# Optimization experiments

Hardware: AMD Instinct MI355X
Metric: run time of the kernel (lower is better)

## Reference

```python
import jax, jax.numpy as jnp
import numpy as np

BS = 4
N_NODES = 10000
N_FEAT = 64
HID = 128
N_LAYERS = 4
HID_FC = 512
N_CLASSES = 10
N_EDGES = 160000


def setup_inputs() -> dict:
    key = jax.random.key(0)
    ks = jax.random.split(key, 10)
    x = jax.random.normal(ks[0], (BS, N_NODES, N_FEAT), jnp.float32)
    edge_index = jax.random.randint(ks[1], (2, N_EDGES), 0, N_NODES, dtype=jnp.int32)
    # batch[b*N_NODES + i] = b, matching x.view(num_nodes*bs, -1) row-major flatten
    batch = jnp.repeat(jnp.arange(BS, dtype=jnp.int32), N_NODES)
    W1 = jax.random.normal(ks[2], (N_FEAT, HID), jnp.float32) * (N_FEAT ** -0.5)
    b1 = jax.random.normal(ks[3], (HID,), jnp.float32) * 0.01
    Ws = jax.random.normal(ks[4], (N_LAYERS - 1, HID, HID), jnp.float32) * (HID ** -0.5)
    bconvs = jax.random.normal(ks[5], (N_LAYERS - 1, HID), jnp.float32) * 0.01
    lin1_w = jax.random.normal(ks[6], (N_LAYERS * HID, HID_FC), jnp.float32) * ((N_LAYERS * HID) ** -0.5)
    lin1_b = jax.random.normal(ks[7], (HID_FC,), jnp.float32) * 0.01
    lin2_w = jax.random.normal(ks[8], (HID_FC, N_CLASSES), jnp.float32) * (HID_FC ** -0.5)
    lin2_b = jax.random.normal(ks[9], (N_CLASSES,), jnp.float32) * 0.01
    return {"x": x, "edge_index": edge_index, "batch": batch,
            "W1": W1, "b1": b1, "Ws": Ws, "bconvs": bconvs,
            "lin1_w": lin1_w, "lin1_b": lin1_b, "lin2_w": lin2_w, "lin2_b": lin2_b}


def _gcn_norm(edge_index, n):
    # PyG GCNConv: add self-loops, symmetric normalization D^-1/2 (A+I) D^-1/2
    loops = jnp.arange(n, dtype=edge_index.dtype)
    src = jnp.concatenate([edge_index[0], loops])
    dst = jnp.concatenate([edge_index[1], loops])
    deg = jnp.zeros((n,), jnp.float32).at[dst].add(1.0)
    dinv = jnp.where(deg > 0, jax.lax.rsqrt(deg), 0.0)
    return src, dst, dinv[src] * dinv[dst]


def reference(x, edge_index, batch, W1, b1, Ws, bconvs, lin1_w, lin1_b, lin2_w, lin2_b):
    bs, n, _ = x.shape
    src, dst, norm = _gcn_norm(edge_index, n)

    def gcn(h, W, b):
        m = (h @ W)[:, src, :] * norm[None, :, None]          # [bs, E+n, H]
        agg = jax.vmap(lambda mm: jax.ops.segment_sum(mm, dst, num_segments=n))(m)
        return agg + b

    h = jax.nn.relu(gcn(x, W1, b1))
    xs = [h]
    for i in range(Ws.shape[0]):
        h = jax.nn.relu(gcn(h, Ws[i], bconvs[i]))
        xs.append(h)
    # torch.stack(xs, -1).view(bs, n, -1): per-channel layer interleave
    h = jnp.stack(xs, -1).reshape(bs, n, -1)                   # [bs, n, L*H]
    flat = h.reshape(bs * n, -1)
    summed = jax.ops.segment_sum(flat, batch, num_segments=bs)
    counts = jax.ops.segment_sum(jnp.ones((bs * n,), flat.dtype), batch, num_segments=bs)
    pooled = summed / counts[:, None]                          # global_mean_pool
    h = jax.nn.relu(pooled @ lin1_w + lin1_b)
    # dropout p=0.5 is inference-disabled (training=False)
    logits = h @ lin2_w + lin2_b
    return jax.nn.log_softmax(logits, axis=-1)
```

## Files before the change

### kernel.cpp

```cpp
#include <hip/hip_runtime.h>
#include <hip/hip_bf16.h>
#include <math.h>

#define N_NODES 10000
#define N_EDGES 160000
#define BS      4
#define N_TOT   (BS * N_NODES)
#define HID     128
#define NPC     4
#define CHUNKS  (N_NODES/NPC)
#define SLOTS   2500
#define HID_FC  512
#define N_CLASSES 10
#define N_LAYERS  4
#define DEG_CAP 64
#define ZERO_INT4 325000

using bf16x8 = __attribute__((ext_vector_type(8))) short;
using f32x4  = __attribute__((ext_vector_type(4))) float;
using f32x2  = __attribute__((ext_vector_type(2))) float;

__device__ __forceinline__ unsigned bf_rne(float x) {
    unsigned b = __float_as_uint(x);
    return (b + 0x7fffu + ((b >> 16) & 1u)) >> 16;
}
__device__ __forceinline__ float bf2f(unsigned hi16) { return __uint_as_float(hi16 << 16); }

#if __has_builtin(__builtin_amdgcn_cvt_pk_f32_fp8) && __has_builtin(__builtin_amdgcn_cvt_pk_fp8_f32)
#define HW_FP8 1
#else
#define HW_FP8 0
#endif

__device__ __forceinline__ float fp8_dec1(unsigned b) {
    unsigned s = (b & 0x80u) << 24;
    unsigned em = b & 0x7Fu;
    float mag;
    if (em >= 8u) mag = __uint_as_float((((em >> 3) + 120u) << 23) | ((em & 7u) << 20));
    else          mag = (float)em * 0x1p-9f;
    return __uint_as_float(s | __float_as_uint(mag));
}

__device__ __forceinline__ unsigned fp8_enc(float x) {
#if HW_FP8
    return (unsigned)(__builtin_amdgcn_cvt_pk_fp8_f32(x, x, 0, false) & 0xFF);
#else
    unsigned s = (__float_as_uint(x) >> 24) & 0x80u;
    float ax = fabsf(x);
    unsigned r;
    if (ax >= 0x1p-6f) {
        if (ax > 448.f) r = 0x7Eu;
        else {
            unsigned b = __float_as_uint(ax);
            unsigned t = b + 0x7FFFFu + ((b >> 20) & 1u);
            r = (t >> 20) - 960u;
        }
    } else {
        r = (unsigned)__float2int_rn(ax * 512.f);
    }
    return s | r;
#endif
}

__device__ __forceinline__ void fp8x8_dec(uint2 u, float* f) {
#if HW_FP8
    f32x2 p0 = __builtin_amdgcn_cvt_pk_f32_fp8((int)u.x, false);
    f32x2 p1 = __builtin_amdgcn_cvt_pk_f32_fp8((int)u.x, true);
    f32x2 p2 = __builtin_amdgcn_cvt_pk_f32_fp8((int)u.y, false);
    f32x2 p3 = __builtin_amdgcn_cvt_pk_f32_fp8((int)u.y, true);
    f[0] = p0[0]; f[1] = p0[1]; f[2] = p1[0]; f[3] = p1[1];
    f[4] = p2[0]; f[5] = p2[1]; f[6] = p3[0]; f[7] = p3[1];
#else
    f[0] = fp8_dec1(u.x & 0xFFu);         f[1] = fp8_dec1((u.x >> 8) & 0xFFu);
    f[2] = fp8_dec1((u.x >> 16) & 0xFFu); f[3] = fp8_dec1((u.x >> 24) & 0xFFu);
    f[4] = fp8_dec1(u.y & 0xFFu);         f[5] = fp8_dec1((u.y >> 8) & 0xFFu);
    f[6] = fp8_dec1((u.y >> 16) & 0xFFu); f[7] = fp8_dec1((u.y >> 24) & 0xFFu);
#endif
}

__device__ __forceinline__ void agg_node(const uint2* __restrict__ tin,
                                         const int* __restrict__ counts,
                                         const int2* __restrict__ csr,
                                         int n, int l, const float* bvv, float* r) {
    int cnt = counts[n];
    const float dn = rsqrtf((float)(cnt + 1));
    if (cnt > DEG_CAP) cnt = DEG_CAP;
    const int no = (cnt + 7) >> 3;
    float acc[8];
    {
        uint2 us = tin[n * 64 + l];
        float sf[8];
        fp8x8_dec(us, sf);
        #pragma unroll
        for (int j = 0; j < 8; ++j) acc[j] = dn * sf[j];
    }
    const int4* cp = (const int4*)(csr + ((size_t)n << 6));
    for (int q = 0; q < no; ++q) {
        int4 q0 = cp[4 * q], q1 = cp[4 * q + 1], q2 = cp[4 * q + 2], q3 = cp[4 * q + 3];
        uint2 u0 = tin[q0.x * 64 + l];
        uint2 u1 = tin[q0.z * 64 + l];
        uint2 u2 = tin[q1.x * 64 + l];
        uint2 u3 = tin[q1.z * 64 + l];
        uint2 u4 = tin[q2.x * 64 + l];
        uint2 u5 = tin[q2.z * 64 + l];
        uint2 u6 = tin[q3.x * 64 + l];
        uint2 u7 = tin[q3.z * 64 + l];
        float w0 = __int_as_float(q0.y), w1 = __int_as_float(q0.w);
        float w2 = __int_as_float(q1.y), w3 = __int_as_float(q1.w);
        float w4 = __int_as_float(q2.y), w5 = __int_as_float(q2.w);
        float w6 = __int_as_float(q3.y), w7 = __int_as_float(q3.w);
        float f[8];
        fp8x8_dec(u0, f);
        #pragma unroll
        for (int j = 0; j < 8; ++j) acc[j] = fmaf(w0, f[j], acc[j]);
        fp8x8_dec(u1, f);
        #pragma unroll
        for (int j = 0; j < 8; ++j) acc[j] = fmaf(w1, f[j], acc[j]);
        fp8x8_dec(u2, f);
        #pragma unroll
        for (int j = 0; j < 8; ++j) acc[j] = fmaf(w2, f[j], acc[j]);
        fp8x8_dec(u3, f);
        #pragma unroll
        for (int j = 0; j < 8; ++j) acc[j] = fmaf(w3, f[j], acc[j]);
        fp8x8_dec(u4, f);
        #pragma unroll
        for (int j = 0; j < 8; ++j) acc[j] = fmaf(w4, f[j], acc[j]);
        fp8x8_dec(u5, f);
        #pragma unroll
        for (int j = 0; j < 8; ++j) acc[j] = fmaf(w5, f[j], acc[j]);
        fp8x8_dec(u6, f);
        #pragma unroll
        for (int j = 0; j < 8; ++j) acc[j] = fmaf(w6, f[j], acc[j]);
        fp8x8_dec(u7, f);
        #pragma unroll
        for (int j = 0; j < 8; ++j) acc[j] = fmaf(w7, f[j], acc[j]);
    }
    #pragma unroll
    for (int j = 0; j < 8; ++j)
        r[j] = fmaxf(fmaf(dn, acc[j], bvv[j]), 0.f);
}

__global__ __launch_bounds__(256) void k_prep(const float* __restrict__ x,
                                              const float* __restrict__ W1,
                                              const float* __restrict__ Ws,
                                              int4* __restrict__ zbase,
                                              ushort* __restrict__ x_bf,
                                              ushort* __restrict__ wt_hi,
                                              ushort* __restrict__ wt_lo) {
    const int gt = blockIdx.x * 256 + threadIdx.x, NT = gridDim.x * 256;
    for (int i = gt; i < ZERO_INT4; i += NT) zbase[i] = make_int4(0, 0, 0, 0);
    for (int i = gt; i < 640000; i += NT) {
        float4 v = ((const float4*)x)[i];
        ushort4 o;
        o.x = (ushort)bf_rne(v.x); o.y = (ushort)bf_rne(v.y);
        o.z = (ushort)bf_rne(v.z); o.w = (ushort)bf_rne(v.w);
        ((ushort4*)x_bf)[i] = o;
    }
    for (int i = gt; i < 57344; i += NT) {
        float v;
        if (i < 8192) { int c = i >> 6, k = i & 63; v = W1[k * HID + c]; }
        else {
            int tt = i - 8192, li = tt >> 14, rem = tt & 16383;
            int c = rem >> 7, k = rem & 127;
            v = Ws[li * 16384 + k * HID + c];
        }
        unsigned hi = bf_rne(v);
        unsigned lo = bf_rne(v - bf2f(hi));
        wt_hi[i] = (ushort)hi;
        wt_lo[i] = (ushort)lo;
    }
}

__global__ void k_count(const int* __restrict__ ei, int* __restrict__ counts) {
    int e = blockIdx.x * 256 + threadIdx.x;
    if (e < N_EDGES) atomicAdd(&counts[ei[N_EDGES + e]], 1);
}

__global__ void k_fill(const int* __restrict__ ei, const int* __restrict__ counts,
                       int* __restrict__ cursor, int2* __restrict__ csr) {
    int e = blockIdx.x * 256 + threadIdx.x;
    if (e < N_EDGES) {
        int s = ei[e], d = ei[N_EDGES + e];
        float ws = rsqrtf((float)(counts[s] + 1));
        int pos = atomicAdd(&cursor[d], 1);
        if (pos < DEG_CAP)
            csr[(d << 6) + pos] = make_int2(s, __float_as_int(ws));
    }
}

template<int K>
__global__ __launch_bounds__(256) void k_mm(const ushort* __restrict__ A,
                                            const ushort* __restrict__ Bt_hi,
                                            const ushort* __restrict__ Bt_lo,
                                            unsigned char* __restrict__ outF8) {
    constexpr int NS = K / 32;
    const int lane = threadIdx.x & 63;
    const int w    = threadIdx.x >> 6;
    const int row_base = blockIdx.x * 128 + w * 32;
    const int lr = lane & 15, lg = lane >> 4;

    bf16x8 a[2][NS];
    #pragma unroll
    for (int rh = 0; rh < 2; ++rh) {
        int r = row_base + rh * 16 + lr;
        if (r > N_TOT - 1) r = N_TOT - 1;
        const ushort* ap = A + (size_t)r * K + lg * 8;
        #pragma unroll
        for (int s = 0; s < NS; ++s)
            a[rh][s] = *(const bf16x8*)(ap + s * 32);
    }

    f32x4 acc[2][8];
    #pragma unroll
    for (int rh = 0; rh < 2; ++rh)
        #pragma unroll
        for (int n = 0; n < 8; ++n)
            acc[rh][n] = (f32x4){0.f, 0.f, 0.f, 0.f};

    #pragma unroll
    for (int n = 0; n < 8; ++n) {
        const ushort* bp = Bt_hi + (size_t)(n * 16 + lr) * K + lg * 8;
        const ushort* bq = Bt_lo + (size_t)(n * 16 + lr) * K + lg * 8;
        #pragma unroll
        for (int s = 0; s < NS; ++s) {
            bf16x8 bh = *(const bf16x8*)(bp + s * 32);
            bf16x8 bl = *(const bf16x8*)(bq + s * 32);
            acc[0][n] = __builtin_amdgcn_mfma_f32_16x16x32_bf16(a[0][s], bh, acc[0][n], 0, 0, 0);
            acc[1][n] = __builtin_amdgcn_mfma_f32_16x16x32_bf16(a[1][s], bh, acc[1][n], 0, 0, 0);
            acc[0][n] = __builtin_amdgcn_mfma_f32_16x16x32_bf16(a[0][s], bl, acc[0][n], 0, 0, 0);
            acc[1][n] = __builtin_amdgcn_mfma_f32_16x16x32_bf16(a[1][s], bl, acc[1][n], 0, 0, 0);
        }
    }

    #pragma unroll
    for (int rh = 0; rh < 2; ++rh) {
        int rb = row_base + rh * 16 + lg * 4;
        #pragma unroll
        for (int n = 0; n < 8; ++n) {
            int col = n * 16 + lr;
            #pragma unroll
            for (int j = 0; j < 4; ++j) {
                int r = rb + j;
                if (r < N_TOT) {
                    int b = r / N_NODES;
                    int nd = r - b * N_NODES;
                    outF8[(size_t)nd * 512 + b * 128 + col] =
                        (unsigned char)fp8_enc(acc[rh][n][j]);
                }
            }
        }
    }
}

__global__ __launch_bounds__(256) void k_fused_am(const uint2* __restrict__ tin,
                                                  const int* __restrict__ counts,
                                                  const int2* __restrict__ csr,
                                                  const float* __restrict__ bias,
                                                  const ushort* __restrict__ Bt_hi,
                                                  const ushort* __restrict__ Bt_lo,
                                                  unsigned char* __restrict__ tout,
                                                  float* __restrict__ partial_l) {
    __shared__ ushort Al[64 * 128];
    __shared__ float pw[4][64][8];
    const int t = threadIdx.x;
    const int w = t >> 6, l = t & 63;
    const int b = l >> 4, ci = l & 15, c0 = ci * 8;
    const int nd0 = blockIdx.x * 16;

    float bvv[8];
    {
        float4 b0 = *(const float4*)(bias + c0);
        float4 b1 = *(const float4*)(bias + c0 + 4);
        bvv[0] = b0.x; bvv[1] = b0.y; bvv[2] = b0.z; bvv[3] = b0.w;
        bvv[4] = b1.x; bvv[5] = b1.y; bvv[6] = b1.z; bvv[7] = b1.w;
    }
    float pool[8];
    #pragma unroll
    for (int j = 0; j < 8; ++j) pool[j] = 0.f;

    for (int ni = 0; ni < 4; ++ni) {
        const int n = nd0 + w * 4 + ni;
        float r[8];
        agg_node(tin, counts, csr, n, l, bvv, r);
        #pragma unroll
        for (int j = 0; j < 8; ++j) pool[j] += r[j];
        const int row = ((w * 4 + ni) << 2) + b;
        unsigned off = (unsigned)(row * 256 + ci * 16);
        off ^= (unsigned)((row & 7) << 4);
        uint4 ov;
        ov.x = bf_rne(r[0]) | (bf_rne(r[1]) << 16);
        ov.y = bf_rne(r[2]) | (bf_rne(r[3]) << 16);
        ov.z = bf_rne(r[4]) | (bf_rne(r[5]) << 16);
        ov.w = bf_rne(r[6]) | (bf_rne(r[7]) << 16);
        *(uint4*)((char*)Al + off) = ov;
    }
    #pragma unroll
    for (int j = 0; j < 8; ++j) pw[w][l][j] = pool[j];
    __syncthreads();

    if (w == 0) {
        float s[8];
        #pragma unroll
        for (int j = 0; j < 8; ++j)
            s[j] = pw[0][l][j] + pw[1][l][j] + pw[2][l][j] + pw[3][l][j];
        float* pp = partial_l + ((size_t)b * SLOTS + blockIdx.x) * HID + c0;
        *(float4*)pp = make_float4(s[0], s[1], s[2], s[3]);
        *(float4*)(pp + 4) = make_float4(s[4], s[5], s[6], s[7]);
    }

    const int lr = l & 15, lg = l >> 4;
    bf16x8 a[4];
    {
        const int row = w * 16 + lr;
        #pragma unroll
        for (int s = 0; s < 4; ++s) {
            unsigned off = (unsigned)(row * 256 + lg * 16 + s * 64);
            off ^= (unsigned)((row & 7) << 4);
            a[s] = *(const bf16x8*)((const char*)Al + off);
        }
    }

    f32x4 acc[8];
    #pragma unroll
    for (int n = 0; n < 8; ++n) acc[n] = (f32x4){0.f, 0.f, 0.f, 0.f};
    #pragma unroll
    for (int n = 0; n < 8; ++n) {
        const ushort* bp = Bt_hi + (size_t)(n * 16 + lr) * 128 + lg * 8;
        const ushort* bq = Bt_lo + (size_t)(n * 16 + lr) * 128 + lg * 8;
        #pragma unroll
        for (int s = 0; s < 4; ++s) {
            bf16x8 bh = *(const bf16x8*)(bp + s * 32);
            bf16x8 bl = *(const bf16x8*)(bq + s * 32);
            acc[n] = __builtin_amdgcn_mfma_f32_16x16x32_bf16(a[s], bh, acc[n], 0, 0, 0);
            acc[n] = __builtin_amdgcn_mfma_f32_16x16x32_bf16(a[s], bl, acc[n], 0, 0, 0);
        }
    }

    #pragma unroll
    for (int n = 0; n < 8; ++n) {
        const int col = n * 16 + lr;
        #pragma unroll
        for (int j = 0; j < 4; ++j) {
            const int row = w * 16 + lg * 4 + j;
            const int nd = nd0 + (row >> 2), bb = row & 3;
            tout[(size_t)nd * 512 + bb * 128 + col] = (unsigned char)fp8_enc(acc[n][j]);
        }
    }
}

__global__ __launch_bounds__(128) void k_agg_last(const uint2* __restrict__ tin,
                                                  const int* __restrict__ counts,
                                                  const int2* __restrict__ csr,
                                                  const float* __restrict__ bias,
                                                  float* __restrict__ partial_l) {
    const int chunk = blockIdx.x;
    const int w = threadIdx.x >> 6, l = threadIdx.x & 63;
    const int b = l >> 4, c0 = (l & 15) * 8;
    float bvv[8];
    {
        float4 b0 = *(const float4*)(bias + c0);
        float4 b1 = *(const float4*)(bias + c0 + 4);
        bvv[0] = b0.x; bvv[1] = b0.y; bvv[2] = b0.z; bvv[3] = b0.w;
        bvv[4] = b1.x; bvv[5] = b1.y; bvv[6] = b1.z; bvv[7] = b1.w;
    }
    float pool[8];
    #pragma unroll
    for (int j = 0; j < 8; ++j) pool[j] = 0.f;
    const int n0 = chunk * NPC + w * (NPC / 2);
    for (int n = n0; n < n0 + NPC / 2; ++n) {
        float r[8];
        agg_node(tin, counts, csr, n, l, bvv, r);
        #pragma unroll
        for (int j = 0; j < 8; ++j) pool[j] += r[j];
    }
    __shared__ float pw[64][8];
    if (w == 1) {
        #pragma unroll
        for (int j = 0; j < 8; ++j) pw[l][j] = pool[j];
    }
    __syncthreads();
    if (w == 0) {
        #pragma unroll
        for (int j = 0; j < 8; ++j) pool[j] += pw[l][j];
        float* pp = partial_l + ((size_t)b * SLOTS + chunk) * HID + c0;
        *(float4*)pp = make_float4(pool[0], pool[1], pool[2], pool[3]);
        *(float4*)(pp + 4) = make_float4(pool[4], pool[5], pool[6], pool[7]);
    }
}

__global__ __launch_bounds__(128) void k_red1(const float* __restrict__ partial,
                                              float* __restrict__ partial2) {
    const int bid = blockIdx.x;
    const int lb = bid >> 5, s = bid & 31;
    const int c = threadIdx.x;
    const int nslots = (lb < 12) ? 625 : SLOTS;
    const int per = (nslots + 31) >> 5;
    const int e0 = s * per;
    int e1 = e0 + per;
    if (e1 > nslots) e1 = nslots;
    const float* p = partial + (size_t)lb * SLOTS * HID + c;
    float sum = 0.f;
    for (int ch = e0; ch < e1; ++ch) sum += p[(size_t)ch * HID];
    partial2[(size_t)bid * HID + c] = sum;
}

__global__ __launch_bounds__(256) void k_lin1(const float* __restrict__ partial2,
                                              const float* __restrict__ w,
                                              const float* __restrict__ bias,
                                              float* __restrict__ h1) {
    __shared__ float pooled_s[16 * HID];
    __shared__ float pf[BS][HID_FC];
    __shared__ float red[8][32][BS];
    const int t = threadIdx.x;
    for (int i = t; i < 16 * HID; i += 256) {
        const float* p = partial2 + (size_t)(i >> 7) * 32 * HID + (i & 127);
        float s = 0.f;
        #pragma unroll
        for (int q = 0; q < 32; ++q) s += p[q * HID];
        pooled_s[i] = s * (1.0f / N_NODES);
    }
    __syncthreads();
    for (int i = t; i < BS * HID_FC; i += 256) {
        int b = i >> 9, f = i & 511;
        int ly = f & 3, cc = f >> 2;
        pf[b][f] = pooled_s[(ly * 4 + b) * HID + cc];
    }
    __syncthreads();
    const int o = t & 31, kq = t >> 5;
    const int o0 = blockIdx.x * 32;
    float acc[BS] = {0.f, 0.f, 0.f, 0.f};
    #pragma unroll 4
    for (int k = kq * 64; k < kq * 64 + 64; ++k) {
        float wv = w[(size_t)k * HID_FC + o0 + o];
        #pragma unroll
        for (int b = 0; b < BS; ++b) acc[b] = fmaf(pf[b][k], wv, acc[b]);
    }
    #pragma unroll
    for (int b = 0; b < BS; ++b) red[kq][o][b] = acc[b];
    __syncthreads();
    if (t < 128) {
        int oo = t & 31, b = t >> 5;
        float s = 0.f;
        #pragma unroll
        for (int q = 0; q < 8; ++q) s += red[q][oo][b];
        s += bias[o0 + oo];
        h1[(size_t)b * HID_FC + o0 + oo] = fmaxf(s, 0.f);
    }
}

__global__ __launch_bounds__(512) void k_lin2(const float* __restrict__ h1,
                                              const float* __restrict__ w,
                                              const float* __restrict__ bias,
                                              float* __restrict__ out) {
    const int k = threadIdx.x;
    const int lane = k & 63, wv_id = k >> 6;
    float wrow[N_CLASSES];
    #pragma unroll
    for (int c = 0; c < N_CLASSES; ++c) wrow[c] = w[k * N_CLASSES + c];
    float hv[BS];
    #pragma unroll
    for (int b = 0; b < BS; ++b) hv[b] = h1[b * HID_FC + k];
    float acc[BS][N_CLASSES];
    #pragma unroll
    for (int b = 0; b < BS; ++b)
        #pragma unroll
        for (int c = 0; c < N_CLASSES; ++c) acc[b][c] = hv[b] * wrow[c];
    #pragma unroll
    for (int off = 32; off >= 1; off >>= 1) {
        #pragma unroll
        for (int b = 0; b < BS; ++b)
            #pragma unroll
            for (int c = 0; c < N_CLASSES; ++c)
                acc[b][c] += __shfl_down(acc[b][c], off);
    }
    __shared__ float red[8][BS * N_CLASSES];
    if (lane == 0) {
        #pragma unroll
        for (int b = 0; b < BS; ++b)
            #pragma unroll
            for (int c = 0; c < N_CLASSES; ++c)
                red[wv_id][b * N_CLASSES + c] = acc[b][c];
    }
    __syncthreads();
    __shared__ float logits[BS][N_CLASSES];
    if (k < BS * N_CLASSES) {
        int b = k / N_CLASSES, c = k % N_CLASSES;
        float s = bias[c];
        #pragma unroll
        for (int q = 0; q < 8; ++q) s += red[q][k];
        logits[b][c] = s;
    }
    __syncthreads();
    if (k < BS) {
        float m = logits[k][0];
        for (int i = 1; i < N_CLASSES; ++i) m = fmaxf(m, logits[k][i]);
        float s = 0.f;
        for (int i = 0; i < N_CLASSES; ++i) s += expf(logits[k][i] - m);
        float lse = m + logf(s);
        for (int i = 0; i < N_CLASSES; ++i) out[k * N_CLASSES + i] = logits[k][i] - lse;
    }
}

extern "C" void kernel_launch(void* const* d_in, const int* in_sizes, int n_in,
                              void* d_out, int out_size, void* d_ws, size_t ws_size,
                              hipStream_t stream) {
    const float* x       = (const float*)d_in[0];
    const int*   ei      = (const int*)d_in[1];
    const float* W1      = (const float*)d_in[3];
    const float* b1      = (const float*)d_in[4];
    const float* Ws      = (const float*)d_in[5];
    const float* bconvs  = (const float*)d_in[6];
    const float* lin1_w  = (const float*)d_in[7];
    const float* lin1_b  = (const float*)d_in[8];
    const float* lin2_w  = (const float*)d_in[9];
    const float* lin2_b  = (const float*)d_in[10];
    float* out = (float*)d_out;

    char* base = (char*)d_ws;
    unsigned char* tmpA = (unsigned char*)base; base += (size_t)N_NODES * 512;
    unsigned char* tmpB = (unsigned char*)base; base += (size_t)N_NODES * 512;
    ushort* x_bf   = (ushort*)base;    base += (size_t)N_TOT * 64 * 2;
    ushort* wt_hi  = (ushort*)base;    base += 57344 * 2;
    ushort* wt_lo  = (ushort*)base;    base += 57344 * 2;
    float*  h1     = (float*)base;     base += BS * HID_FC * 4;
    float*  partial  = (float*)base;   base += (size_t)16 * SLOTS * HID * 4;
    float*  partial2 = (float*)base;   base += (size_t)16 * 32 * HID * 4;
    int*    counts = (int*)base;       base += N_NODES * 4;
    int*    cursor = (int*)base;       base += N_NODES * 4;
    int2*   csr    = (int2*)base;

    const int GE = (N_EDGES + 255) / 256;
    const int mm_grid = (N_TOT + 127) / 128;

    k_prep<<<1024, 256, 0, stream>>>(x, W1, Ws, (int4*)counts, x_bf, wt_hi, wt_lo);
    k_count<<<GE, 256, 0, stream>>>(ei, counts);
    k_fill<<<GE, 256, 0, stream>>>(ei, counts, cursor, csr);

    k_mm<64><<<mm_grid, 256, 0, stream>>>(x_bf, wt_hi, wt_lo, tmpA);

    unsigned char* tin = tmpA;
    unsigned char* tou = tmpB;
    for (int j = 0; j < 3; ++j) {
        const float* bj = (j == 0) ? b1 : (bconvs + (size_t)(j - 1) * HID);
        const ushort* whi = wt_hi + 8192 + (size_t)j * 16384;
        const ushort* wlo = wt_lo + 8192 + (size_t)j * 16384;
        k_fused_am<<<N_NODES / 16, 256, 0, stream>>>((const uint2*)tin, counts, csr, bj,
                                                     whi, wlo, tou,
                                                     partial + (size_t)j * 4 * SLOTS * HID);
        unsigned char* tswap = tin; tin = tou; tou = tswap;
    }

    k_agg_last<<<CHUNKS, 128, 0, stream>>>((const uint2*)tin, counts, csr,
                                           bconvs + 2 * HID,
                                           partial + (size_t)3 * 4 * SLOTS * HID);

    k_red1<<<16 * 32, 128, 0, stream>>>(partial, partial2);
    k_lin1<<<HID_FC / 32, 256, 0, stream>>>(partial2, lin1_w, lin1_b, h1);
    k_lin2<<<1, 512, 0, stream>>>(h1, lin2_w, lin2_b, out);
}
```

Baseline: 220.9 us.

## Fuse x bf16 conversion into first matmul and widen aggregation blocks

Drops the separate fp32-to-bf16 pass over x in the prep kernel and converts x to bf16 inside the first MFMA matmul, which removes a full write and re-read of the bf16 copy. The fused aggregate-matmul kernel moves to 512 threads, with each wave aggregating 2 nodes instead of 4 and the 64x128 MFMA tile split across 8 waves (2 column halves). The last aggregation kernel uses 4 waves with one node each. Together these raise parallelism per block for the latency-bound gather, at the cost of more LDS per block and possibly lower occupancy.

```diff
diff --git a/kernel.cpp b/kernel.cpp
--- a/kernel.cpp
+++ b/kernel.cpp
@@ -7,12 +7,10 @@
 #define BS      4
 #define N_TOT   (BS * N_NODES)
 #define HID     128
-#define NPC     4
-#define CHUNKS  (N_NODES/NPC)
+#define CHUNKS  2500
 #define SLOTS   2500
 #define HID_FC  512
 #define N_CLASSES 10
-#define N_LAYERS  4
 #define DEG_CAP 64
 #define ZERO_INT4 325000
 
@@ -140,22 +138,13 @@
         r[j] = fmaxf(fmaf(dn, acc[j], bvv[j]), 0.f);
 }
 
-__global__ __launch_bounds__(256) void k_prep(const float* __restrict__ x,
-                                              const float* __restrict__ W1,
+__global__ __launch_bounds__(256) void k_prep(const float* __restrict__ W1,
                                               const float* __restrict__ Ws,
                                               int4* __restrict__ zbase,
-                                              ushort* __restrict__ x_bf,
                                               ushort* __restrict__ wt_hi,
                                               ushort* __restrict__ wt_lo) {
     const int gt = blockIdx.x * 256 + threadIdx.x, NT = gridDim.x * 256;
     for (int i = gt; i < ZERO_INT4; i += NT) zbase[i] = make_int4(0, 0, 0, 0);
-    for (int i = gt; i < 640000; i += NT) {
-        float4 v = ((const float4*)x)[i];
-        ushort4 o;
-        o.x = (ushort)bf_rne(v.x); o.y = (ushort)bf_rne(v.y);
-        o.z = (ushort)bf_rne(v.z); o.w = (ushort)bf_rne(v.w);
-        ((ushort4*)x_bf)[i] = o;
-    }
     for (int i = gt; i < 57344; i += NT) {
         float v;
         if (i < 8192) { int c = i >> 6, k = i & 63; v = W1[k * HID + c]; }
@@ -188,26 +177,32 @@
     }
 }
 
-template<int K>
-__global__ __launch_bounds__(256) void k_mm(const ushort* __restrict__ A,
-                                            const ushort* __restrict__ Bt_hi,
-                                            const ushort* __restrict__ Bt_lo,
-                                            unsigned char* __restrict__ outF8) {
-    constexpr int NS = K / 32;
+__global__ __launch_bounds__(256) void k_mm64(const float* __restrict__ X,
+                                              const ushort* __restrict__ Bt_hi,
+                                              const ushort* __restrict__ Bt_lo,
+                                              unsigned char* __restrict__ outF8) {
     const int lane = threadIdx.x & 63;
     const int w    = threadIdx.x >> 6;
     const int row_base = blockIdx.x * 128 + w * 32;
     const int lr = lane & 15, lg = lane >> 4;
 
-    bf16x8 a[2][NS];
+    bf16x8 a[2][2];
     #pragma unroll
     for (int rh = 0; rh < 2; ++rh) {
         int r = row_base + rh * 16 + lr;
         if (r > N_TOT - 1) r = N_TOT - 1;
-        const ushort* ap = A + (size_t)r * K + lg * 8;
-        #pragma unroll
-        for (int s = 0; s < NS; ++s)
-            a[rh][s] = *(const bf16x8*)(ap + s * 32);
+        const float* ap = X + (size_t)r * 64 + lg * 8;
+        #pragma unroll
+        for (int s = 0; s < 2; ++s) {
+            float4 v0 = *(const float4*)(ap + s * 32);
+            float4 v1 = *(const float4*)(ap + s * 32 + 4);
+            union { bf16x8 v; ushort u[8]; } cv;
+            cv.u[0] = (ushort)bf_rne(v0.x); cv.u[1] = (ushort)bf_rne(v0.y);
+            cv.u[2] = (ushort)bf_rne(v0.z); cv.u[3] = (ushort)bf_rne(v0.w);
+            cv.u[4] = (ushort)bf_rne(v1.x); cv.u[5] = (ushort)bf_rne(v1.y);
+            cv.u[6] = (ushort)bf_rne(v1.z); cv.u[7] = (ushort)bf_rne(v1.w);
+            a[rh][s] = cv.v;
+        }
     }
 
     f32x4 acc[2][8];
@@ -219,10 +214,10 @@
 
     #pragma unroll
     for (int n = 0; n < 8; ++n) {
-        const ushort* bp = Bt_hi + (size_t)(n * 16 + lr) * K + lg * 8;
-        const ushort* bq = Bt_lo + (size_t)(n * 16 + lr) * K + lg * 8;
-        #pragma unroll
-        for (int s = 0; s < NS; ++s) {
+        const ushort* bp = Bt_hi + (size_t)(n * 16 + lr) * 64 + lg * 8;
+        const ushort* bq = Bt_lo + (size_t)(n * 16 + lr) * 64 + lg * 8;
+        #pragma unroll
+        for (int s = 0; s < 2; ++s) {
             bf16x8 bh = *(const bf16x8*)(bp + s * 32);
             bf16x8 bl = *(const bf16x8*)(bq + s * 32);
             acc[0][n] = __builtin_amdgcn_mfma_f32_16x16x32_bf16(a[0][s], bh, acc[0][n], 0, 0, 0);
@@ -252,7 +247,7 @@
     }
 }
 
-__global__ __launch_bounds__(256) void k_fused_am(const uint2* __restrict__ tin,
+__global__ __launch_bounds__(512) void k_fused_am(const uint2* __restrict__ tin,
                                                   const int* __restrict__ counts,
                                                   const int2* __restrict__ csr,
                                                   const float* __restrict__ bias,
@@ -261,7 +256,7 @@
                                                   unsigned char* __restrict__ tout,
                                                   float* __restrict__ partial_l) {
     __shared__ ushort Al[64 * 128];
-    __shared__ float pw[4][64][8];
+    __shared__ float pw[8][64][8];
     const int t = threadIdx.x;
     const int w = t >> 6, l = t & 63;
     const int b = l >> 4, ci = l & 15, c0 = ci * 8;
@@ -278,13 +273,14 @@
     #pragma unroll
     for (int j = 0; j < 8; ++j) pool[j] = 0.f;
 
-    for (int ni = 0; ni < 4; ++ni) {
-        const int n = nd0 + w * 4 + ni;
+    #pragma unroll
+    for (int ni = 0; ni < 2; ++ni) {
+        const int n = nd0 + w * 2 + ni;
         float r[8];
         agg_node(tin, counts, csr, n, l, bvv, r);
         #pragma unroll
         for (int j = 0; j < 8; ++j) pool[j] += r[j];
-        const int row = ((w * 4 + ni) << 2) + b;
+        const int row = ((w * 2 + ni) << 2) + b;
         unsigned off = (unsigned)(row * 256 + ci * 16);
         off ^= (unsigned)((row & 7) << 4);
         uint4 ov;
@@ -301,17 +297,21 @@
     if (w == 0) {
         float s[8];
         #pragma unroll
-        for (int j = 0; j < 8; ++j)
-            s[j] = pw[0][l][j] + pw[1][l][j] + pw[2][l][j] + pw[3][l][j];
+        for (int j = 0; j < 8; ++j) {
+            s[j] = 0.f;
+            #pragma unroll
+            for (int q = 0; q < 8; ++q) s[j] += pw[q][l][j];
+        }
         float* pp = partial_l + ((size_t)b * SLOTS + blockIdx.x) * HID + c0;
         *(float4*)pp = make_float4(s[0], s[1], s[2], s[3]);
         *(float4*)(pp + 4) = make_float4(s[4], s[5], s[6], s[7]);
     }
 
+    const int wr = w >> 1, wc = w & 1;
     const int lr = l & 15, lg = l >> 4;
     bf16x8 a[4];
     {
-        const int row = w * 16 + lr;
+        const int row = wr * 16 + lr;
         #pragma unroll
         for (int s = 0; s < 4; ++s) {
             unsigned off = (unsigned)(row * 256 + lg * 16 + s * 64);
@@ -320,13 +320,14 @@
         }
     }
 
-    f32x4 acc[8];
-    #pragma unroll
-    for (int n = 0; n < 8; ++n) acc[n] = (f32x4){0.f, 0.f, 0.f, 0.f};
-    #pragma unroll
-    for (int n = 0; n < 8; ++n) {
-        const ushort* bp = Bt_hi + (size_t)(n * 16 + lr) * 128 + lg * 8;
-        const ushort* bq = Bt_lo + (size_t)(n * 16 + lr) * 128 + lg * 8;
+    f32x4 acc[4];
+    #pragma unroll
+    for (int n = 0; n < 4; ++n) acc[n] = (f32x4){0.f, 0.f, 0.f, 0.f};
+    #pragma unroll
+    for (int n = 0; n < 4; ++n) {
+        const int col = wc * 64 + n * 16 + lr;
+        const ushort* bp = Bt_hi + (size_t)col * 128 + lg * 8;
+        const ushort* bq = Bt_lo + (size_t)col * 128 + lg * 8;
         #pragma unroll
         for (int s = 0; s < 4; ++s) {
             bf16x8 bh = *(const bf16x8*)(bp + s * 32);
@@ -337,18 +338,18 @@
     }
 
     #pragma unroll
-    for (int n = 0; n < 8; ++n) {
-        const int col = n * 16 + lr;
+    for (int n = 0; n < 4; ++n) {
+        const int col = wc * 64 + n * 16 + lr;
         #pragma unroll
         for (int j = 0; j < 4; ++j) {
-            const int row = w * 16 + lg * 4 + j;
+            const int row = wr * 16 + lg * 4 + j;
             const int nd = nd0 + (row >> 2), bb = row & 3;
             tout[(size_t)nd * 512 + bb * 128 + col] = (unsigned char)fp8_enc(acc[n][j]);
         }
     }
 }
 
-__global__ __launch_bounds__(128) void k_agg_last(const uint2* __restrict__ tin,
+__global__ __launch_bounds__(256) void k_agg_last(const uint2* __restrict__ tin,
                                                   const int* __restrict__ counts,
                                                   const int2* __restrict__ csr,
                                                   const float* __restrict__ bias,
@@ -363,25 +364,17 @@
         bvv[0] = b0.x; bvv[1] = b0.y; bvv[2] = b0.z; bvv[3] = b0.w;
         bvv[4] = b1.x; bvv[5] = b1.y; bvv[6] = b1.z; bvv[7] = b1.w;
     }
-    float pool[8];
-    #pragma unroll
-    for (int j = 0; j < 8; ++j) pool[j] = 0.f;
-    const int n0 = chunk * NPC + w * (NPC / 2);
-    for (int n = n0; n < n0 + NPC / 2; ++n) {
-        float r[8];
-        agg_node(tin, counts, csr, n, l, bvv, r);
-        #pragma unroll
-        for (int j = 0; j < 8; ++j) pool[j] += r[j];
-    }
-    __shared__ float pw[64][8];
-    if (w == 1) {
-        #pragma unroll
-        for (int j = 0; j < 8; ++j) pw[l][j] = pool[j];
-    }
+    float r[8];
+    agg_node(tin, counts, csr, chunk * 4 + w, l, bvv, r);
+    __shared__ float pw[4][64][8];
+    #pragma unroll
+    for (int j = 0; j < 8; ++j) pw[w][l][j] = r[j];
     __syncthreads();
     if (w == 0) {
-        #pragma unroll
-        for (int j = 0; j < 8; ++j) pool[j] += pw[l][j];
+        float pool[8];
+        #pragma unroll
+        for (int j = 0; j < 8; ++j)
+            pool[j] = pw[0][l][j] + pw[1][l][j] + pw[2][l][j] + pw[3][l][j];
         float* pp = partial_l + ((size_t)b * SLOTS + chunk) * HID + c0;
         *(float4*)pp = make_float4(pool[0], pool[1], pool[2], pool[3]);
         *(float4*)(pp + 4) = make_float4(pool[4], pool[5], pool[6], pool[7]);
@@ -519,7 +512,6 @@
     char* base = (char*)d_ws;
     unsigned char* tmpA = (unsigned char*)base; base += (size_t)N_NODES * 512;
     unsigned char* tmpB = (unsigned char*)base; base += (size_t)N_NODES * 512;
-    ushort* x_bf   = (ushort*)base;    base += (size_t)N_TOT * 64 * 2;
     ushort* wt_hi  = (ushort*)base;    base += 57344 * 2;
     ushort* wt_lo  = (ushort*)base;    base += 57344 * 2;
     float*  h1     = (float*)base;     base += BS * HID_FC * 4;
@@ -532,11 +524,11 @@
     const int GE = (N_EDGES + 255) / 256;
     const int mm_grid = (N_TOT + 127) / 128;
 
-    k_prep<<<1024, 256, 0, stream>>>(x, W1, Ws, (int4*)counts, x_bf, wt_hi, wt_lo);
+    k_prep<<<512, 256, 0, stream>>>(W1, Ws, (int4*)counts, wt_hi, wt_lo);
     k_count<<<GE, 256, 0, stream>>>(ei, counts);
     k_fill<<<GE, 256, 0, stream>>>(ei, counts, cursor, csr);
 
-    k_mm<64><<<mm_grid, 256, 0, stream>>>(x_bf, wt_hi, wt_lo, tmpA);
+    k_mm64<<<mm_grid, 256, 0, stream>>>(x, wt_hi, wt_lo, tmpA);
 
     unsigned char* tin = tmpA;
     unsigned char* tou = tmpB;
@@ -544,13 +536,13 @@
         const float* bj = (j == 0) ? b1 : (bconvs + (size_t)(j - 1) * HID);
         const ushort* whi = wt_hi + 8192 + (size_t)j * 16384;
         const ushort* wlo = wt_lo + 8192 + (size_t)j * 16384;
-        k_fused_am<<<N_NODES / 16, 256, 0, stream>>>((const uint2*)tin, counts, csr, bj,
+        k_fused_am<<<N_NODES / 16, 512, 0, stream>>>((const uint2*)tin, counts, csr, bj,
                                                      whi, wlo, tou,
                                                      partial + (size_t)j * 4 * SLOTS * HID);
         unsigned char* tswap = tin; tin = tou; tou = tswap;
     }
 
-    k_agg_last<<<CHUNKS, 128, 0, stream>>>((const uint2*)tin, counts, csr,
+    k_agg_last<<<CHUNKS, 256, 0, stream>>>((const uint2*)tin, counts, csr,
                                            bconvs + 2 * HID,
                                            partial + (size_t)3 * 4 * SLOTS * HID);
 
```

New measurement: 221.1 us (median of 2 runs). About the same (+0.1%).
